# Kernel tuning notes

Measured on AMD Instinct MI355X. Metric: run time of the kernel, lower is better.

Reference implementation:

```python
import jax, jax.numpy as jnp
import numpy as np

V, D, N, S = 100000, 256, 8192, 20
H = D  # hidden size == feat_dim (nn.LSTM(feat_dim, feat_dim))


def setup_inputs() -> dict:
    key = jax.random.key(0)
    ks = jax.random.split(key, 8)
    sc = 1.0 / np.sqrt(H)  # PyTorch LSTM default init scale
    return {
        "emb": jax.random.normal(ks[0], (V, D), jnp.float32),
        "w_ih_f": jax.random.normal(ks[1], (4 * H, D), jnp.float32) * sc,
        "w_hh_f": jax.random.normal(ks[2], (4 * H, H), jnp.float32) * sc,
        "b_f": jax.random.normal(ks[3], (4 * H,), jnp.float32) * sc,
        "w_ih_b": jax.random.normal(ks[4], (4 * H, D), jnp.float32) * sc,
        "w_hh_b": jax.random.normal(ks[5], (4 * H, H), jnp.float32) * sc,
        "b_b": jax.random.normal(ks[6], (4 * H,), jnp.float32) * sc,
        "neigh_idx": jax.random.randint(ks[7], (N, S), 0, V, dtype=jnp.int64),
    }


def _lstm_dir(x, w_ih, w_hh, b):
    """Batched unidirectional LSTM. x: [N, S, D] -> hidden states [N, S, H].
    PyTorch gate order: i, f, g, o."""
    h_dim = w_hh.shape[1]
    # precompute input contribution for all steps: [N, S, 4H]
    xg = jnp.einsum('nsd,gd->nsg', x, w_ih) + b

    def step(carry, xt):
        h, c = carry
        g = xt + h @ w_hh.T
        i, f, gg, o = jnp.split(g, 4, axis=-1)
        c = jax.nn.sigmoid(f) * c + jax.nn.sigmoid(i) * jnp.tanh(gg)
        h = jax.nn.sigmoid(o) * jnp.tanh(c)
        return (h, c), h

    n = x.shape[0]
    init = (jnp.zeros((n, h_dim), x.dtype), jnp.zeros((n, h_dim), x.dtype))
    _, hs = jax.lax.scan(step, init, jnp.swapaxes(xg, 0, 1))  # [S, N, H]
    return jnp.swapaxes(hs, 0, 1)


def reference(emb, w_ih_f, w_hh_f, b_f, w_ih_b, w_hh_b, b_b, neigh_idx):
    x = emb[neigh_idx]  # gather neighbor embeddings: [N, S, D]
    hf = _lstm_dir(x, w_ih_f, w_hh_f, b_f)                      # [N, S, H]
    hb = _lstm_dir(x[:, ::-1, :], w_ih_b, w_hh_b, b_b)[:, ::-1, :]
    h = jnp.concatenate([hf, hb], axis=-1)  # [N, S, 2H]
    summed = h.sum(axis=1)                  # sum over time: [N, 2H]
    # faithful to original: torch.mean over the 1-D summed vector -> scalar
    # broadcast into the full output row
    row = summed.mean(axis=-1, keepdims=True)  # [N, 1]
    return jnp.broadcast_to(row, summed.shape)  # [N, 2H]
```

## Files before the change

### kernel.cpp

```cpp
#include <hip/hip_runtime.h>

#define NN 8192
#define SS 20
#define DD 256
#define RGATE 1024
#define KKD 512

typedef __attribute__((ext_vector_type(8))) short short8;
typedef __attribute__((ext_vector_type(4))) float f32x4;

__device__ __forceinline__ unsigned short f2bf(float f) {
    unsigned int u = __float_as_uint(f);
    u += 0x7FFFu + ((u >> 16) & 1u);
    return (unsigned short)(u >> 16);
}

__device__ __forceinline__ void async_copy16(const void* g, void* l) {
    __builtin_amdgcn_global_load_lds(
        (const __attribute__((address_space(1))) void*)g,
        (__attribute__((address_space(3))) void*)l, 16, 0, 0);
}

__device__ __forceinline__ float sigm(float x) { return 1.0f / (1.0f + __expf(-x)); }
__device__ __forceinline__ float tanh_(float x) { return 2.0f / (1.0f + __expf(-2.0f * x)) - 1.0f; }

__global__ void convert_w(const float* __restrict__ wihf, const float* __restrict__ whhf,
                          const float* __restrict__ bf,   const float* __restrict__ wihb,
                          const float* __restrict__ whhb, const float* __restrict__ bb,
                          unsigned short* __restrict__ Wcat, float* __restrict__ bperm) {
    const int idx = blockIdx.x * 256 + threadIdx.x;
    const int dir = idx >> 19;
    const int rem = idx & ((1 << 19) - 1);
    const int rp  = rem >> 9;
    const int k   = rem & 511;
    const int j   = rp >> 2, gi = rp & 3;
    const int r   = gi * 256 + j;
    const float* wih = dir ? wihb : wihf;
    const float* whh = dir ? whhb : whhf;
    const float v = (k < 256) ? wih[r * 256 + k] : whh[r * 256 + (k - 256)];
    Wcat[idx] = f2bf(v);
    if (k == 0) {
        const float* b = dir ? bb : bf;
        bperm[dir * 1024 + rp] = b[r];
    }
}

__global__ __launch_bounds__(256) void gather_x(const float* __restrict__ emb,
                                                const int* __restrict__ idx,
                                                unsigned short* __restrict__ X) {
    const int w = threadIdx.x >> 6, lane = threadIdx.x & 63;
    #pragma unroll 4
    for (int i = 0; i < 16; ++i) {
        const int rid = (blockIdx.x * 16 + i) * 4 + w;
        const int n = rid / SS, t = rid - n * SS;
        const int row = idx[rid];
        const float4 v = ((const float4*)(emb + (size_t)row * DD))[lane];
        ushort4 o;
        o.x = f2bf(v.x); o.y = f2bf(v.y); o.z = f2bf(v.z); o.w = f2bf(v.w);
        ((ushort4*)(X + ((size_t)t * NN + n) * DD))[lane] = o;
    }
}

__global__ __launch_bounds__(512, 2) void lstm_step(
    const unsigned short* __restrict__ X,
    const unsigned short* __restrict__ Wcat,
    const float* __restrict__ bperm,
    unsigned short* __restrict__ hping,
    float* __restrict__ cstate,
    float* __restrict__ hsum,
    int s) {
    const int b     = blockIdx.x;
    const int dir   = b & 1;
    const int nblk  = (b >> 3) & 3;
    const int mslab = (((b & 7) >> 1) << 3) | (b >> 5);
    const int m0    = mslab * 256;
    const int n0    = nblk * 256;

    const int t = dir ? (SS - 1 - s) : s;
    const unsigned short* Xt    = X + (size_t)t * NN * DD;
    const unsigned short* hprev = hping + ((size_t)((s & 1) * 2 + dir)) * NN * 256;
    unsigned short*       hnext = hping + ((size_t)((((s + 1) & 1) * 2) + dir)) * NN * 256;
    const unsigned short* W     = Wcat + (size_t)dir * RGATE * KKD;
    const float*          bp    = bperm + dir * RGATE;
    float*                cdir  = cstate + (size_t)dir * NN * 256;

    __shared__ __align__(16) char smem[98304];

    const int tid  = threadIdx.x;
    const int lane = tid & 63;
    const int w    = tid >> 6;
    const int wm   = w >> 1, wn = w & 1;
    const int quad = lane >> 4, l15 = lane & 15;
    const int jq   = lane & 3,  rl  = lane >> 2;

    const int srow  = lane >> 2;
    const int gsegl = (lane & 3) ^ ((lane >> 3) & 3);

    auto stage = [&](int rr, int buf) {
        const int k0 = (rr & 7) * 32;
        const unsigned short* Asrc = (rr < 8) ? Xt : hprev;
        char* Ad = smem + buf * 16384;
        char* Bd = smem + 49152 + buf * 16384;
        #pragma unroll
        for (int i = 0; i < 2; ++i) {
            const int lr = w * 32 + i * 16 + srow;
            async_copy16(Asrc + (size_t)(m0 + lr) * DD + k0 + gsegl * 8,
                         (void*)(Ad + (w * 32 + i * 16) * 64));
            async_copy16(W + (size_t)(n0 + lr) * KKD + rr * 32 + gsegl * 8,
                         (void*)(Bd + (w * 32 + i * 16) * 64));
        }
    };

    f32x4 acc[4][8];
    #pragma unroll
    for (int i = 0; i < 4; ++i)
        #pragma unroll
        for (int j = 0; j < 8; ++j) acc[i][j] = f32x4{0.f, 0.f, 0.f, 0.f};

    const int sA = (quad ^ ((l15 >> 1) & 3)) * 16;

    auto krnd = [&](int cb) {
        const char* Ab = smem + cb * 16384;
        const char* Bb = smem + 49152 + cb * 16384;
        short8 af[4], bfr[8];
        #pragma unroll
        for (int mt = 0; mt < 4; ++mt)
            af[mt] = *(const short8*)(Ab + (wm * 64 + mt * 16 + l15) * 64 + sA);
        #pragma unroll
        for (int nt = 0; nt < 8; ++nt)
            bfr[nt] = *(const short8*)(Bb + (wn * 128 + nt * 16 + l15) * 64 + sA);
        #pragma unroll
        for (int mt = 0; mt < 4; ++mt)
            #pragma unroll
            for (int nt = 0; nt < 8; ++nt)
                acc[mt][nt] = __builtin_amdgcn_mfma_f32_16x16x32_bf16(
                    af[mt], bfr[nt], acc[mt][nt], 0, 0, 0);
    };

    stage(0, 0);
    stage(1, 1);
    {
        int cb = 0, sb = 2;
        #pragma unroll
        for (int r = 0; r < 14; ++r) {
            asm volatile("s_waitcnt vmcnt(4)" ::: "memory");
            asm volatile("s_barrier" ::: "memory");
            krnd(cb);
            stage(r + 2, sb);
            cb = (cb == 2) ? 0 : cb + 1;
            sb = (sb == 2) ? 0 : sb + 1;
        }
        asm volatile("s_waitcnt vmcnt(4)" ::: "memory");
        asm volatile("s_barrier" ::: "memory");
        krnd(2);
        asm volatile("s_waitcnt vmcnt(0)" ::: "memory");
        asm volatile("s_barrier" ::: "memory");
        krnd(0);
        asm volatile("s_barrier" ::: "memory");
    }

    float* my = (float*)smem + w * 1088;
    float hs[4] = {0.f, 0.f, 0.f, 0.f};

    #pragma unroll
    for (int half = 0; half < 2; ++half) {
        const int j0 = nblk * 64 + wn * 32 + half * 16 + jq * 4;
        f32x4 bias4[4];
        #pragma unroll
        for (int jj = 0; jj < 4; ++jj)
            bias4[jj] = *(const f32x4*)(bp + 4 * (j0 + jj));
        #pragma unroll
        for (int mt = 0; mt < 4; ++mt) {
            #pragma unroll
            for (int nt = 0; nt < 4; ++nt) {
                const int ntg = half * 4 + nt;
                #pragma unroll
                for (int v = 0; v < 4; ++v)
                    my[(quad * 4 + v) * 68 + nt * 16 + l15] = acc[mt][ntg][v];
            }
            asm volatile("s_waitcnt lgkmcnt(0)" ::: "memory");
            const int mg = m0 + wm * 64 + mt * 16 + rl;
            float* cptr = cdir + (size_t)mg * 256 + j0;
            f32x4 cold = *(const f32x4*)cptr;
            f32x4 cnew;
            ushort4 hp;
            float lsum = 0.f;
            #pragma unroll
            for (int jj = 0; jj < 4; ++jj) {
                f32x4 g  = *(const f32x4*)(my + rl * 68 + (jq * 4 + jj) * 4);
                f32x4 bb = bias4[jj];
                const float gi = sigm(g.x + bb.x);
                const float gf = sigm(g.y + bb.y);
                const float gg = tanh_(g.z + bb.z);
                const float go = sigm(g.w + bb.w);
                const float cn = gf * cold[jj] + gi * gg;
                cnew[jj] = cn;
                const float hv = go * tanh_(cn);
                lsum += hv;
                ((unsigned short*)&hp)[jj] = f2bf(hv);
            }
            *(f32x4*)cptr = cnew;
            *(ushort4*)(hnext + (size_t)mg * 256 + j0) = hp;
            hs[mt] += lsum;
        }
    }

    #pragma unroll
    for (int mt = 0; mt < 4; ++mt) {
        float v = hs[mt];
        v += __shfl_xor(v, 1);
        v += __shfl_xor(v, 2);
        if (jq == 0) atomicAdd(&hsum[m0 + wm * 64 + mt * 16 + rl], v);
    }
}

__global__ void bcast_out(const float* __restrict__ hsum, float* __restrict__ out) {
    const int n = blockIdx.x;
    const float v = hsum[n] * (1.0f / 512.0f);
    float2 p; p.x = v; p.y = v;
    ((float2*)(out + (size_t)n * 512))[threadIdx.x] = p;
}

extern "C" void kernel_launch(void* const* d_in, const int* in_sizes, int n_in,
                              void* d_out, int out_size, void* d_ws, size_t ws_size,
                              hipStream_t stream) {
    const float* emb  = (const float*)d_in[0];
    const float* wihf = (const float*)d_in[1];
    const float* whhf = (const float*)d_in[2];
    const float* bf   = (const float*)d_in[3];
    const float* wihb = (const float*)d_in[4];
    const float* whhb = (const float*)d_in[5];
    const float* bb   = (const float*)d_in[6];
    const int*   idx  = (const int*)d_in[7];
    float* out = (float*)d_out;

    char* ws = (char*)d_ws;
    unsigned short* X     = (unsigned short*)(ws);
    unsigned short* Wcat  = (unsigned short*)(ws + 83886080);
    float*          bperm = (float*)(ws + 85983232);
    unsigned short* hping = (unsigned short*)(ws + 85991424);
    float*          cst   = (float*)(ws + 102768640);
    float*          hsum  = (float*)(ws + 119545856);

    hipMemsetAsync(hping, 0, 8388608, stream);
    hipMemsetAsync(cst, 0, 16777216 + 32768, stream);

    convert_w<<<4096, 256, 0, stream>>>(wihf, whhf, bf, wihb, whhb, bb, Wcat, bperm);
    gather_x<<<2560, 256, 0, stream>>>(emb, idx, X);
    for (int s = 0; s < SS; ++s)
        lstm_step<<<256, 512, 0, stream>>>(X, Wcat, bperm, hping, cst, hsum, s);
    bcast_out<<<NN, 256, 0, stream>>>(hsum, out);
}
```

Baseline: 745.6 us.

## Fuse per-timestep LSTM launches into one persistent kernel with flag sync

Replaces 20 separate lstm_step launches with a single persistent kernel that loops over timesteps. Blocks working on the same row slab and direction sync through per-step atomic counters. Each block waits on the previous step's flag only before it stages the recurrent h part, so the input-projection rounds overlap with other blocks finishing. The first step skips the h-part rounds and the c-state load, which lets the memsets of h and c be dropped. This relies on all 256 blocks being co-resident (2 per CU), otherwise the spin-waits deadlock.

```diff
diff --git a/kernel.cpp b/kernel.cpp
--- a/kernel.cpp
+++ b/kernel.cpp
@@ -61,14 +61,14 @@
     }
 }
 
-__global__ __launch_bounds__(512, 2) void lstm_step(
+__global__ __launch_bounds__(512, 2) void lstm_persist(
     const unsigned short* __restrict__ X,
     const unsigned short* __restrict__ Wcat,
     const float* __restrict__ bperm,
     unsigned short* __restrict__ hping,
     float* __restrict__ cstate,
     float* __restrict__ hsum,
-    int s) {
+    unsigned int* __restrict__ flags) {
     const int b     = blockIdx.x;
     const int dir   = b & 1;
     const int nblk  = (b >> 3) & 3;
@@ -76,13 +76,10 @@
     const int m0    = mslab * 256;
     const int n0    = nblk * 256;
 
-    const int t = dir ? (SS - 1 - s) : s;
-    const unsigned short* Xt    = X + (size_t)t * NN * DD;
-    const unsigned short* hprev = hping + ((size_t)((s & 1) * 2 + dir)) * NN * 256;
-    unsigned short*       hnext = hping + ((size_t)((((s + 1) & 1) * 2) + dir)) * NN * 256;
-    const unsigned short* W     = Wcat + (size_t)dir * RGATE * KKD;
-    const float*          bp    = bperm + dir * RGATE;
-    float*                cdir  = cstate + (size_t)dir * NN * 256;
+    const unsigned short* W  = Wcat + (size_t)dir * RGATE * KKD;
+    const float*          bp = bperm + dir * RGATE;
+    float*                cdir = cstate + (size_t)dir * NN * 256;
+    unsigned int*         myflags = flags + (dir * 32 + mslab) * SS;
 
     __shared__ __align__(16) char smem[98304];
 
@@ -96,28 +93,9 @@
     const int srow  = lane >> 2;
     const int gsegl = (lane & 3) ^ ((lane >> 3) & 3);
 
-    auto stage = [&](int rr, int buf) {
-        const int k0 = (rr & 7) * 32;
-        const unsigned short* Asrc = (rr < 8) ? Xt : hprev;
-        char* Ad = smem + buf * 16384;
-        char* Bd = smem + 49152 + buf * 16384;
-        #pragma unroll
-        for (int i = 0; i < 2; ++i) {
-            const int lr = w * 32 + i * 16 + srow;
-            async_copy16(Asrc + (size_t)(m0 + lr) * DD + k0 + gsegl * 8,
-                         (void*)(Ad + (w * 32 + i * 16) * 64));
-            async_copy16(W + (size_t)(n0 + lr) * KKD + rr * 32 + gsegl * 8,
-                         (void*)(Bd + (w * 32 + i * 16) * 64));
-        }
-    };
+    const int sA = (quad ^ ((l15 >> 1) & 3)) * 16;
 
     f32x4 acc[4][8];
-    #pragma unroll
-    for (int i = 0; i < 4; ++i)
-        #pragma unroll
-        for (int j = 0; j < 8; ++j) acc[i][j] = f32x4{0.f, 0.f, 0.f, 0.f};
-
-    const int sA = (quad ^ ((l15 >> 1) & 3)) * 16;
 
     auto krnd = [&](int cb) {
         const char* Ab = smem + cb * 16384;
@@ -137,80 +115,115 @@
                     af[mt], bfr[nt], acc[mt][nt], 0, 0, 0);
     };
 
-    stage(0, 0);
-    stage(1, 1);
-    {
+    for (int s = 0; s < SS; ++s) {
+        const int t = dir ? (SS - 1 - s) : s;
+        const unsigned short* Xt    = X + (size_t)t * NN * DD;
+        const unsigned short* hprev = hping + ((size_t)((s & 1) * 2 + dir)) * NN * 256;
+        unsigned short*       hnext = hping + ((size_t)((((s + 1) & 1) * 2) + dir)) * NN * 256;
+        const int nr = s ? 16 : 8;
+
+        auto stage = [&](int rr, int buf) {
+            const int k0 = (rr & 7) * 32;
+            const unsigned short* Asrc = (rr < 8) ? Xt : hprev;
+            char* Ad = smem + buf * 16384;
+            char* Bd = smem + 49152 + buf * 16384;
+            #pragma unroll
+            for (int i = 0; i < 2; ++i) {
+                const int lr = w * 32 + i * 16 + srow;
+                async_copy16(Asrc + (size_t)(m0 + lr) * DD + k0 + gsegl * 8,
+                             (void*)(Ad + (w * 32 + i * 16) * 64));
+                async_copy16(W + (size_t)(n0 + lr) * KKD + rr * 32 + gsegl * 8,
+                             (void*)(Bd + (w * 32 + i * 16) * 64));
+            }
+        };
+
+        #pragma unroll
+        for (int i = 0; i < 4; ++i)
+            #pragma unroll
+            for (int j = 0; j < 8; ++j) acc[i][j] = f32x4{0.f, 0.f, 0.f, 0.f};
+
+        stage(0, 0);
+        stage(1, 1);
         int cb = 0, sb = 2;
-        #pragma unroll
-        for (int r = 0; r < 14; ++r) {
-            asm volatile("s_waitcnt vmcnt(4)" ::: "memory");
+        for (int r = 0; r < nr; ++r) {
+            if (r + 1 < nr) { asm volatile("s_waitcnt vmcnt(4)" ::: "memory"); }
+            else            { asm volatile("s_waitcnt vmcnt(0)" ::: "memory"); }
             asm volatile("s_barrier" ::: "memory");
             krnd(cb);
-            stage(r + 2, sb);
+            if (r + 2 < nr) {
+                if (r == 6 && s) {
+                    const unsigned int* fl = myflags + (s - 1);
+                    while (__hip_atomic_load(fl, __ATOMIC_ACQUIRE,
+                                             __HIP_MEMORY_SCOPE_AGENT) != 4u)
+                        __builtin_amdgcn_s_sleep(2);
+                }
+                stage(r + 2, sb);
+            }
             cb = (cb == 2) ? 0 : cb + 1;
             sb = (sb == 2) ? 0 : sb + 1;
         }
-        asm volatile("s_waitcnt vmcnt(4)" ::: "memory");
         asm volatile("s_barrier" ::: "memory");
-        krnd(2);
-        asm volatile("s_waitcnt vmcnt(0)" ::: "memory");
-        asm volatile("s_barrier" ::: "memory");
-        krnd(0);
-        asm volatile("s_barrier" ::: "memory");
-    }
-
-    float* my = (float*)smem + w * 1088;
-    float hs[4] = {0.f, 0.f, 0.f, 0.f};
-
-    #pragma unroll
-    for (int half = 0; half < 2; ++half) {
-        const int j0 = nblk * 64 + wn * 32 + half * 16 + jq * 4;
-        f32x4 bias4[4];
-        #pragma unroll
-        for (int jj = 0; jj < 4; ++jj)
-            bias4[jj] = *(const f32x4*)(bp + 4 * (j0 + jj));
+
+        float* my = (float*)smem + w * 1088;
+        float hs[4] = {0.f, 0.f, 0.f, 0.f};
+
+        #pragma unroll
+        for (int half = 0; half < 2; ++half) {
+            const int j0 = nblk * 64 + wn * 32 + half * 16 + jq * 4;
+            f32x4 bias4[4];
+            #pragma unroll
+            for (int jj = 0; jj < 4; ++jj)
+                bias4[jj] = *(const f32x4*)(bp + 4 * (j0 + jj));
+            #pragma unroll
+            for (int mt = 0; mt < 4; ++mt) {
+                #pragma unroll
+                for (int nt = 0; nt < 4; ++nt) {
+                    const int ntg = half * 4 + nt;
+                    #pragma unroll
+                    for (int v = 0; v < 4; ++v)
+                        my[(quad * 4 + v) * 68 + nt * 16 + l15] = acc[mt][ntg][v];
+                }
+                asm volatile("s_waitcnt lgkmcnt(0)" ::: "memory");
+                const int mg = m0 + wm * 64 + mt * 16 + rl;
+                float* cptr = cdir + (size_t)mg * 256 + j0;
+                f32x4 cold;
+                if (s) cold = *(const f32x4*)cptr;
+                else   cold = f32x4{0.f, 0.f, 0.f, 0.f};
+                f32x4 cnew;
+                ushort4 hp;
+                float lsum = 0.f;
+                #pragma unroll
+                for (int jj = 0; jj < 4; ++jj) {
+                    f32x4 g  = *(const f32x4*)(my + rl * 68 + (jq * 4 + jj) * 4);
+                    f32x4 bb = bias4[jj];
+                    const float gi = sigm(g.x + bb.x);
+                    const float gf = sigm(g.y + bb.y);
+                    const float gg = tanh_(g.z + bb.z);
+                    const float go = sigm(g.w + bb.w);
+                    const float cn = gf * cold[jj] + gi * gg;
+                    cnew[jj] = cn;
+                    const float hv = go * tanh_(cn);
+                    lsum += hv;
+                    ((unsigned short*)&hp)[jj] = f2bf(hv);
+                }
+                *(f32x4*)cptr = cnew;
+                *(ushort4*)(hnext + (size_t)mg * 256 + j0) = hp;
+                hs[mt] += lsum;
+            }
+        }
+
         #pragma unroll
         for (int mt = 0; mt < 4; ++mt) {
-            #pragma unroll
-            for (int nt = 0; nt < 4; ++nt) {
-                const int ntg = half * 4 + nt;
-                #pragma unroll
-                for (int v = 0; v < 4; ++v)
-                    my[(quad * 4 + v) * 68 + nt * 16 + l15] = acc[mt][ntg][v];
-            }
-            asm volatile("s_waitcnt lgkmcnt(0)" ::: "memory");
-            const int mg = m0 + wm * 64 + mt * 16 + rl;
-            float* cptr = cdir + (size_t)mg * 256 + j0;
-            f32x4 cold = *(const f32x4*)cptr;
-            f32x4 cnew;
-            ushort4 hp;
-            float lsum = 0.f;
-            #pragma unroll
-            for (int jj = 0; jj < 4; ++jj) {
-                f32x4 g  = *(const f32x4*)(my + rl * 68 + (jq * 4 + jj) * 4);
-                f32x4 bb = bias4[jj];
-                const float gi = sigm(g.x + bb.x);
-                const float gf = sigm(g.y + bb.y);
-                const float gg = tanh_(g.z + bb.z);
-                const float go = sigm(g.w + bb.w);
-                const float cn = gf * cold[jj] + gi * gg;
-                cnew[jj] = cn;
-                const float hv = go * tanh_(cn);
-                lsum += hv;
-                ((unsigned short*)&hp)[jj] = f2bf(hv);
-            }
-            *(f32x4*)cptr = cnew;
-            *(ushort4*)(hnext + (size_t)mg * 256 + j0) = hp;
-            hs[mt] += lsum;
+            float v = hs[mt];
+            v += __shfl_xor(v, 1);
+            v += __shfl_xor(v, 2);
+            if (jq == 0) atomicAdd(&hsum[m0 + wm * 64 + mt * 16 + rl], v);
         }
-    }
-
-    #pragma unroll
-    for (int mt = 0; mt < 4; ++mt) {
-        float v = hs[mt];
-        v += __shfl_xor(v, 1);
-        v += __shfl_xor(v, 2);
-        if (jq == 0) atomicAdd(&hsum[m0 + wm * 64 + mt * 16 + rl], v);
+
+        __syncthreads();
+        if (tid == 0)
+            __hip_atomic_fetch_add(myflags + s, 1u, __ATOMIC_RELEASE,
+                                   __HIP_MEMORY_SCOPE_AGENT);
     }
 }
 
@@ -241,13 +254,12 @@
     unsigned short* hping = (unsigned short*)(ws + 85991424);
     float*          cst   = (float*)(ws + 102768640);
     float*          hsum  = (float*)(ws + 119545856);
-
-    hipMemsetAsync(hping, 0, 8388608, stream);
-    hipMemsetAsync(cst, 0, 16777216 + 32768, stream);
+    unsigned int*   flags = (unsigned int*)(ws + 119578624);
+
+    hipMemsetAsync(hsum, 0, 32768 + 5120, stream);
 
     convert_w<<<4096, 256, 0, stream>>>(wihf, whhf, bf, wihb, whhb, bb, Wcat, bperm);
     gather_x<<<2560, 256, 0, stream>>>(emb, idx, X);
-    for (int s = 0; s < SS; ++s)
-        lstm_step<<<256, 512, 0, stream>>>(X, Wcat, bperm, hping, cst, hsum, s);
+    lstm_persist<<<256, 512, 0, stream>>>(X, Wcat, bperm, hping, cst, hsum, flags);
     bcast_out<<<NN, 256, 0, stream>>>(hsum, out);
 }
```

Result: slower. 1.110 ms (+48.9%).

## Skip zero h-state GEMM at step 0, split k-round MFMA with prio

Applied to the files above, without the earlier changes.

At the first timestep the recurrent h·W_hh half of the K loop is skipped, because h is zero. The initial cell state is treated as zero in registers instead of being loaded, which lets the large memsets of the h and c buffers be dropped so that only hsum is cleared. The k-round loop is also restructured: B fragments load in two halves, with setprio and sched_barrier around the MFMA groups and an extra barrier per round. This lowers register pressure and aims at better overlap, at the cost of a runtime loop and more synchronization.

```diff
diff --git a/kernel.cpp b/kernel.cpp
--- a/kernel.cpp
+++ b/kernel.cpp
@@ -96,6 +96,8 @@
     const int srow  = lane >> 2;
     const int gsegl = (lane & 3) ^ ((lane >> 3) & 3);
 
+    const int nr = s ? 16 : 8;
+
     auto stage = [&](int rr, int buf) {
         const int k0 = (rr & 7) * 32;
         const unsigned short* Asrc = (rr < 8) ? Xt : hprev;
@@ -119,45 +121,54 @@
 
     const int sA = (quad ^ ((l15 >> 1) & 3)) * 16;
 
-    auto krnd = [&](int cb) {
+    stage(0, 0);
+    stage(1, 1);
+    int cb = 0, sb = 2;
+    for (int r = 0; r < nr; ++r) {
+        if (r + 1 < nr) { asm volatile("s_waitcnt vmcnt(4)" ::: "memory"); }
+        else            { asm volatile("s_waitcnt vmcnt(0)" ::: "memory"); }
+        asm volatile("s_barrier" ::: "memory");
+        __builtin_amdgcn_sched_barrier(0);
         const char* Ab = smem + cb * 16384;
         const char* Bb = smem + 49152 + cb * 16384;
-        short8 af[4], bfr[8];
+        short8 af[4], bfr[4];
         #pragma unroll
         for (int mt = 0; mt < 4; ++mt)
             af[mt] = *(const short8*)(Ab + (wm * 64 + mt * 16 + l15) * 64 + sA);
         #pragma unroll
-        for (int nt = 0; nt < 8; ++nt)
+        for (int nt = 0; nt < 4; ++nt)
             bfr[nt] = *(const short8*)(Bb + (wn * 128 + nt * 16 + l15) * 64 + sA);
+        if (r + 2 < nr) stage(r + 2, sb);
+        asm volatile("s_waitcnt lgkmcnt(0)" ::: "memory");
+        __builtin_amdgcn_sched_barrier(0);
+        __builtin_amdgcn_s_setprio(1);
         #pragma unroll
         for (int mt = 0; mt < 4; ++mt)
             #pragma unroll
-            for (int nt = 0; nt < 8; ++nt)
+            for (int nt = 0; nt < 4; ++nt)
                 acc[mt][nt] = __builtin_amdgcn_mfma_f32_16x16x32_bf16(
                     af[mt], bfr[nt], acc[mt][nt], 0, 0, 0);
-    };
-
-    stage(0, 0);
-    stage(1, 1);
-    {
-        int cb = 0, sb = 2;
-        #pragma unroll
-        for (int r = 0; r < 14; ++r) {
-            asm volatile("s_waitcnt vmcnt(4)" ::: "memory");
-            asm volatile("s_barrier" ::: "memory");
-            krnd(cb);
-            stage(r + 2, sb);
-            cb = (cb == 2) ? 0 : cb + 1;
-            sb = (sb == 2) ? 0 : sb + 1;
-        }
-        asm volatile("s_waitcnt vmcnt(4)" ::: "memory");
+        __builtin_amdgcn_s_setprio(0);
+        __builtin_amdgcn_sched_barrier(0);
         asm volatile("s_barrier" ::: "memory");
-        krnd(2);
-        asm volatile("s_waitcnt vmcnt(0)" ::: "memory");
-        asm volatile("s_barrier" ::: "memory");
-        krnd(0);
-        asm volatile("s_barrier" ::: "memory");
-    }
+        #pragma unroll
+        for (int nt = 0; nt < 4; ++nt)
+            bfr[nt] = *(const short8*)(Bb + (wn * 128 + (nt + 4) * 16 + l15) * 64 + sA);
+        asm volatile("s_waitcnt lgkmcnt(0)" ::: "memory");
+        __builtin_amdgcn_sched_barrier(0);
+        __builtin_amdgcn_s_setprio(1);
+        #pragma unroll
+        for (int mt = 0; mt < 4; ++mt)
+            #pragma unroll
+            for (int nt = 0; nt < 4; ++nt)
+                acc[mt][nt + 4] = __builtin_amdgcn_mfma_f32_16x16x32_bf16(
+                    af[mt], bfr[nt], acc[mt][nt + 4], 0, 0, 0);
+        __builtin_amdgcn_s_setprio(0);
+        __builtin_amdgcn_sched_barrier(0);
+        cb = (cb == 2) ? 0 : cb + 1;
+        sb = (sb == 2) ? 0 : sb + 1;
+    }
+    asm volatile("s_barrier" ::: "memory");
 
     float* my = (float*)smem + w * 1088;
     float hs[4] = {0.f, 0.f, 0.f, 0.f};
@@ -181,7 +192,9 @@
             asm volatile("s_waitcnt lgkmcnt(0)" ::: "memory");
             const int mg = m0 + wm * 64 + mt * 16 + rl;
             float* cptr = cdir + (size_t)mg * 256 + j0;
-            f32x4 cold = *(const f32x4*)cptr;
+            f32x4 cold;
+            if (s) cold = *(const f32x4*)cptr;
+            else   cold = f32x4{0.f, 0.f, 0.f, 0.f};
             f32x4 cnew;
             ushort4 hp;
             float lsum = 0.f;
@@ -242,8 +255,7 @@
     float*          cst   = (float*)(ws + 102768640);
     float*          hsum  = (float*)(ws + 119545856);
 
-    hipMemsetAsync(hping, 0, 8388608, stream);
-    hipMemsetAsync(cst, 0, 16777216 + 32768, stream);
+    hipMemsetAsync(hsum, 0, 32768, stream);
 
     convert_w<<<4096, 256, 0, stream>>>(wihf, whhf, bf, wihb, whhb, bb, Wcat, bperm);
     gather_x<<<2560, 256, 0, stream>>>(emb, idx, X);
```

Result: slower. 826.0 us (+10.8%).

## Skip recurrent GEMM half at first step and deepen LDS pipeline to four buffers

Applied to the files above, without the earlier changes.

At step zero the hidden and cell states are zero, so the kernel runs only the input-projection K rounds and skips loading c. This allows removing the memsets of the h ping-pong and c state buffers, keeping only the hsum clear. The staging pipeline also moves from triple to quadruple buffering with 128KB of LDS and a runtime-bounded loop. The loop is no longer fully unrolled, which may add indexing overhead.

```diff
diff --git a/kernel.cpp b/kernel.cpp
--- a/kernel.cpp
+++ b/kernel.cpp
@@ -84,7 +84,7 @@
     const float*          bp    = bperm + dir * RGATE;
     float*                cdir  = cstate + (size_t)dir * NN * 256;
 
-    __shared__ __align__(16) char smem[98304];
+    __shared__ __align__(16) char smem[131072];
 
     const int tid  = threadIdx.x;
     const int lane = tid & 63;
@@ -96,11 +96,13 @@
     const int srow  = lane >> 2;
     const int gsegl = (lane & 3) ^ ((lane >> 3) & 3);
 
+    const int nr = s ? 16 : 8;
+
     auto stage = [&](int rr, int buf) {
         const int k0 = (rr & 7) * 32;
         const unsigned short* Asrc = (rr < 8) ? Xt : hprev;
         char* Ad = smem + buf * 16384;
-        char* Bd = smem + 49152 + buf * 16384;
+        char* Bd = smem + 65536 + buf * 16384;
         #pragma unroll
         for (int i = 0; i < 2; ++i) {
             const int lr = w * 32 + i * 16 + srow;
@@ -121,7 +123,7 @@
 
     auto krnd = [&](int cb) {
         const char* Ab = smem + cb * 16384;
-        const char* Bb = smem + 49152 + cb * 16384;
+        const char* Bb = smem + 65536 + cb * 16384;
         short8 af[4], bfr[8];
         #pragma unroll
         for (int mt = 0; mt < 4; ++mt)
@@ -139,25 +141,19 @@
 
     stage(0, 0);
     stage(1, 1);
-    {
-        int cb = 0, sb = 2;
-        #pragma unroll
-        for (int r = 0; r < 14; ++r) {
-            asm volatile("s_waitcnt vmcnt(4)" ::: "memory");
-            asm volatile("s_barrier" ::: "memory");
-            krnd(cb);
-            stage(r + 2, sb);
-            cb = (cb == 2) ? 0 : cb + 1;
-            sb = (sb == 2) ? 0 : sb + 1;
-        }
-        asm volatile("s_waitcnt vmcnt(4)" ::: "memory");
+    stage(2, 2);
+    int cb = 0, sb = 3;
+    for (int r = 0; r < nr; ++r) {
+        if (r + 3 <= nr - 1)      { asm volatile("s_waitcnt vmcnt(8)" ::: "memory"); }
+        else if (r + 2 <= nr - 1) { asm volatile("s_waitcnt vmcnt(4)" ::: "memory"); }
+        else                      { asm volatile("s_waitcnt vmcnt(0)" ::: "memory"); }
         asm volatile("s_barrier" ::: "memory");
-        krnd(2);
-        asm volatile("s_waitcnt vmcnt(0)" ::: "memory");
-        asm volatile("s_barrier" ::: "memory");
-        krnd(0);
-        asm volatile("s_barrier" ::: "memory");
-    }
+        krnd(cb);
+        if (r + 3 < nr) stage(r + 3, sb);
+        cb = (cb + 1) & 3;
+        sb = (sb + 1) & 3;
+    }
+    asm volatile("s_barrier" ::: "memory");
 
     float* my = (float*)smem + w * 1088;
     float hs[4] = {0.f, 0.f, 0.f, 0.f};
@@ -181,7 +177,9 @@
             asm volatile("s_waitcnt lgkmcnt(0)" ::: "memory");
             const int mg = m0 + wm * 64 + mt * 16 + rl;
             float* cptr = cdir + (size_t)mg * 256 + j0;
-            f32x4 cold = *(const f32x4*)cptr;
+            f32x4 cold;
+            if (s) cold = *(const f32x4*)cptr;
+            else   cold = f32x4{0.f, 0.f, 0.f, 0.f};
             f32x4 cnew;
             ushort4 hp;
             float lsum = 0.f;
@@ -242,8 +240,7 @@
     float*          cst   = (float*)(ws + 102768640);
     float*          hsum  = (float*)(ws + 119545856);
 
-    hipMemsetAsync(hping, 0, 8388608, stream);
-    hipMemsetAsync(cst, 0, 16777216 + 32768, stream);
+    hipMemsetAsync(hsum, 0, 32768, stream);
 
     convert_w<<<4096, 256, 0, stream>>>(wihf, whhf, bf, wihb, whhb, bb, Wcat, bperm);
     gather_x<<<2560, 256, 0, stream>>>(emb, idx, X);
```

Result: slower. 802.5 us (+7.6%).
